# Kernel optimization log

Hardware: AMD Instinct MI355X
Metric: run time of the kernel (lower is better)

The kernel has to match this reference:

```python
import jax, jax.numpy as jnp
import numpy as np
import math

CTX_LEN = 2048
N_EMB = 256
HEAD_SIZE = 256
N_HEADS = 8
HEAD_DIM = HEAD_SIZE // N_HEADS  # 32
B, T = 4, 2048


def setup_inputs() -> dict:
    key = jax.random.key(0)
    k1, k2, k3, k4 = jax.random.split(key, 4)
    x = jax.random.normal(k1, (B, T, N_EMB), dtype=jnp.float32)
    # torch Linear(n_emb, 3*head_size, bias=False): store as [in, out] for x @ W
    w_attn = jax.random.normal(k2, (N_EMB, 3 * HEAD_SIZE), dtype=jnp.float32) * 0.02
    pos_embs = jax.random.normal(k3, (N_HEADS, CTX_LEN, HEAD_DIM), dtype=jnp.float32) * 0.02
    w_proj = jax.random.normal(k4, (HEAD_SIZE, N_EMB), dtype=jnp.float32) * 0.02
    b_proj = jnp.zeros((N_EMB,), dtype=jnp.float32)
    return {"x": x, "w_attn": w_attn, "pos_embs": pos_embs,
            "w_proj": w_proj, "b_proj": b_proj}


def reference(x, w_attn, pos_embs, w_proj, b_proj):
    Bsz, Tlen, _ = x.shape
    qkv = x @ w_attn                               # [B,T,3*HS]
    K, Q, V = jnp.split(qkv, 3, axis=-1)           # split order: K, Q, V (as in source)
    def heads(t):                                  # [B,T,HS] -> [B,H,T,hd]
        return t.reshape(Bsz, Tlen, N_HEADS, HEAD_DIM).transpose(0, 2, 1, 3)
    K, Q, V = heads(K), heads(Q), heads(V)

    # relative position term with skew trick
    pe = pos_embs[:, -Tlen:, :]                    # [H,T,hd]
    S_rel = jnp.einsum('bhtd,hsd->bhts', Q, pe)    # [B,H,T,T]
    flip_mask = jnp.flip(jnp.tril(jnp.ones((Tlen, Tlen), dtype=x.dtype)), axis=1)
    S_rel = S_rel * flip_mask
    # pad a zero column at the front, reshape [T+1,T], drop first row -> skew
    S_rel = jnp.pad(S_rel, ((0, 0), (0, 0), (0, 0), (1, 0)))
    S_rel = S_rel.reshape(Bsz, N_HEADS, Tlen + 1, Tlen)[:, :, 1:, :]

    scores = (jnp.einsum('bhtd,bhsd->bhts', Q, K) + S_rel) / math.sqrt(HEAD_DIM)
    causal = jnp.where(jnp.tril(jnp.ones((Tlen, Tlen), dtype=bool)), 0.0, -1e9).astype(x.dtype)
    scores = scores + causal
    attn = jax.nn.softmax(scores, axis=-1)         # dropout omitted (eval mode)

    out = jnp.einsum('bhts,bhsd->bhtd', attn, V)   # [B,H,T,hd]
    out = out.transpose(0, 2, 1, 3).reshape(Bsz, Tlen, HEAD_SIZE)
    return out @ w_proj + b_proj
```

## Files before the change

### kernel.cpp

```cpp
#include <hip/hip_runtime.h>
#include <math.h>

#define BB 4
#define TT 2048
#define NEMB 256
#define NH 8
#define HD 32

typedef __attribute__((ext_vector_type(8))) short bf8;
typedef __attribute__((ext_vector_type(4))) float f4;

static __device__ __forceinline__ unsigned short f2bf(float f) {
    union { float f; unsigned u; } v; v.f = f;
    unsigned r = v.u + 0x7FFF + ((v.u >> 16) & 1);
    return (unsigned short)(r >> 16);
}

__global__ __launch_bounds__(256) void xcvt(const float* __restrict__ x,
                                            unsigned short* __restrict__ xb) {
    const long i = (long)blockIdx.x * 256 + threadIdx.x;
    const float4 v = ((const float4*)x)[i];
    ushort4 o; o.x = f2bf(v.x); o.y = f2bf(v.y); o.z = f2bf(v.z); o.w = f2bf(v.w);
    ((ushort4*)xb)[i] = o;
}

__global__ __launch_bounds__(256) void tcvt(const float* __restrict__ src,
                                            unsigned short* __restrict__ dst,
                                            int R, int C) {
    __shared__ float t[64][65];
    const int tid = threadIdx.x;
    const int c0 = blockIdx.x * 64, r0 = blockIdx.y * 64;
    #pragma unroll
    for (int p = 0; p < 4; ++p) {
        const int i = tid + p * 256;
        const int r = i >> 4, c4 = (i & 15) * 4;
        const float4 v = *(const float4*)(src + (long)(r0 + r) * C + c0 + c4);
        t[r][c4] = v.x; t[r][c4+1] = v.y; t[r][c4+2] = v.z; t[r][c4+3] = v.w;
    }
    __syncthreads();
    #pragma unroll
    for (int p = 0; p < 4; ++p) {
        const int i = tid + p * 256;
        const int cr = i >> 4, r4 = (i & 15) * 4;
        ushort4 vv;
        vv.x = f2bf(t[r4+0][cr]); vv.y = f2bf(t[r4+1][cr]);
        vv.z = f2bf(t[r4+2][cr]); vv.w = f2bf(t[r4+3][cr]);
        *(ushort4*)(dst + (long)(c0 + cr) * R + r0 + r4) = vv;
    }
}

__global__ __launch_bounds__(256) void pe_cvt(const float* __restrict__ pe,
                                              unsigned short* __restrict__ peb) {
    const int i = blockIdx.x * 256 + threadIdx.x;
    const float4 v = ((const float4*)pe)[i];
    ushort4 o; o.x = f2bf(v.x); o.y = f2bf(v.y); o.z = f2bf(v.z); o.w = f2bf(v.w);
    ((ushort4*)peb)[i] = o;
}

__global__ __launch_bounds__(256) void qkv_mfma(const unsigned short* __restrict__ Ag,
                                                const unsigned short* __restrict__ Bg,
                                                unsigned short* __restrict__ Kb,
                                                unsigned short* __restrict__ Qb,
                                                unsigned short* __restrict__ Vt) {
    __shared__ unsigned short sm[13824];
    unsigned short* As = sm;
    unsigned short* Bs = sm + 9216;
    const int tid = threadIdx.x;
    const int wv = tid >> 6, L = tid & 63;
    const int l15 = L & 15, q = L >> 4;
    const int n0 = blockIdx.x * 64;
    const int m0 = blockIdx.y * 128;

    f4 acc[2][4];
    #pragma unroll
    for (int mt = 0; mt < 2; ++mt)
        #pragma unroll
        for (int nt = 0; nt < 4; ++nt) acc[mt][nt] = (f4){0.f,0.f,0.f,0.f};

    for (int kc = 0; kc < 4; ++kc) {
        const int k0 = kc * 64;
        __syncthreads();
        #pragma unroll
        for (int p = 0; p < 4; ++p) {
            const int i = tid + p * 256;
            const int r = i >> 3, c = i & 7;
            *(bf8*)(As + r * 72 + c * 8) = *(const bf8*)(Ag + (long)(m0 + r) * 256 + k0 + c * 8);
        }
        #pragma unroll
        for (int p = 0; p < 2; ++p) {
            const int i = tid + p * 256;
            const int r = i >> 3, c = i & 7;
            *(bf8*)(Bs + r * 72 + c * 8) = *(const bf8*)(Bg + (long)(n0 + r) * 256 + k0 + c * 8);
        }
        __syncthreads();
        #pragma unroll
        for (int kk = 0; kk < 2; ++kk) {
            const bf8 a0 = *(const bf8*)(As + (wv * 32 + l15) * 72 + kk * 32 + q * 8);
            const bf8 a1 = *(const bf8*)(As + (wv * 32 + 16 + l15) * 72 + kk * 32 + q * 8);
            #pragma unroll
            for (int nt = 0; nt < 4; ++nt) {
                const bf8 bb = *(const bf8*)(Bs + (nt * 16 + l15) * 72 + kk * 32 + q * 8);
                acc[0][nt] = __builtin_amdgcn_mfma_f32_16x16x32_bf16(a0, bb, acc[0][nt], 0, 0, 0);
                acc[1][nt] = __builtin_amdgcn_mfma_f32_16x16x32_bf16(a1, bb, acc[1][nt], 0, 0, 0);
            }
        }
    }

    const int sec = n0 >> 8;
    #pragma unroll
    for (int mt = 0; mt < 2; ++mt) {
        const int gm = m0 + wv * 32 + mt * 16 + q * 4;
        const int b = gm >> 11, tb = gm & 2047;
        #pragma unroll
        for (int nt = 0; nt < 4; ++nt) {
            const int gn = n0 + nt * 16 + l15;
            const int cc = gn & 255, h = cc >> 5, d = cc & 31;
            const long bh = (long)b * NH + h;
            const f4 a = acc[mt][nt];
            if (sec == 2) {
                ushort4 vv;
                vv.x = f2bf(a[0]); vv.y = f2bf(a[1]); vv.z = f2bf(a[2]); vv.w = f2bf(a[3]);
                *(ushort4*)(Vt + (bh * HD + d) * TT + tb) = vv;
            } else if (sec == 1) {
                #pragma unroll
                for (int r = 0; r < 4; ++r)
                    Qb[(bh * TT + tb + r) * HD + d] = f2bf(a[r] * 0.17677669529663687f);
            } else {
                #pragma unroll
                for (int r = 0; r < 4; ++r)
                    Kb[(bh * TT + tb + r) * HD + d] = f2bf(a[r]);
            }
        }
    }
}

__global__ __launch_bounds__(256) void attn_kernel(const unsigned short* __restrict__ Kb,
                                                   const unsigned short* __restrict__ Qb,
                                                   const unsigned short* __restrict__ Vtg,
                                                   const unsigned short* __restrict__ peb,
                                                   unsigned short* __restrict__ att) {
    __shared__ unsigned short lds[14592];
    unsigned short* Ks  = lds;
    unsigned short* PEs = lds + 2560;
    unsigned short* Vts = lds + 7680;
    unsigned short* Psw = lds + 9984 + (threadIdx.x >> 6) * 1152;

    const int tid = threadIdx.x;
    const int wv  = tid >> 6;
    const int L   = tid & 63;
    const int l15 = L & 15;
    const int q   = L >> 4;
    const int h = blockIdx.y, b = blockIdx.z;
    const long bh = (long)b * NH + h;
    const unsigned short* Kg = Kb  + bh * TT * HD;
    const unsigned short* Qg = Qb  + bh * TT * HD;
    const unsigned short* Vg = Vtg + bh * HD * TT;
    const unsigned short* Pg = peb + (long)h * TT * HD;

    const int krow = tid >> 2, kc = tid & 3;
    const int vrow = tid >> 3, vc = tid & 7;
    const f4 z4 = {0.f, 0.f, 0.f, 0.f};

    for (int half = 0; half < 2; ++half) {
        const int itile = half ? 31 - (int)blockIdx.x : (int)blockIdx.x;
        const int t0 = itile * 64;

        const bf8 aq = *(const bf8*)(Qg + (t0 + wv * 16 + l15) * HD + q * 8);
        f4 o0 = z4, o1 = z4;
        float m_st[4] = {-1e30f, -1e30f, -1e30f, -1e30f};
        float l_st[4] = {0.f, 0.f, 0.f, 0.f};

        for (int jt = 0; jt <= itile; ++jt) {
            const int s0 = jt * 64;
            const int ubase = TT - 64 - t0 + s0;
            __syncthreads();
            *(bf8*)(Ks  + krow * 40 + kc * 8) = *(const bf8*)(Kg + (s0 + krow) * HD + kc * 8);
            *(bf8*)(Vts + vrow * 72 + vc * 8) = *(const bf8*)(Vg + vrow * TT + s0 + vc * 8);
            #pragma unroll
            for (int kk = 0; kk < 2; ++kk) {
                const int i  = tid + kk * 256;
                const int pr = i >> 2, pc = i & 3;
                const int u  = ubase + pr;
                bf8 val = {0,0,0,0,0,0,0,0};
                if (u < TT) val = *(const bf8*)(Pg + (long)u * HD + pc * 8);
                *(bf8*)(PEs + pr * 40 + pc * 8) = val;
            }
            __syncthreads();

            f4 sa[4], ra[5];
            #pragma unroll
            for (int nt = 0; nt < 4; ++nt) {
                const bf8 bk = *(const bf8*)(Ks + (nt * 16 + l15) * 40 + q * 8);
                sa[nt] = __builtin_amdgcn_mfma_f32_16x16x32_bf16(aq, bk, z4, 0, 0, 0);
            }
            const int pebase = 48 - 16 * wv;
            #pragma unroll
            for (int nt = 0; nt < 5; ++nt) {
                const bf8 bp = *(const bf8*)(PEs + (pebase + nt * 16 + l15) * 40 + q * 8);
                ra[nt] = __builtin_amdgcn_mfma_f32_16x16x32_bf16(aq, bp, z4, 0, 0, 0);
            }

            #pragma unroll
            for (int nb = 0; nb < 4; ++nb) {
                #pragma unroll
                for (int r = 0; r < 4; ++r) {
                    const int shift = 15 - 4 * q - r;
                    const int tcol  = l15 + shift;
                    const int src   = (q << 4) | (tcol & 15);
                    const float va = __shfl(ra[nb][r], src);
                    const float vb = __shfl(ra[nb + 1][r], src);
                    sa[nb][r] += (tcol < 16) ? va : vb;
                }
            }

            if (jt == itile) {
                #pragma unroll
                for (int nb = 0; nb < 4; ++nb)
                    #pragma unroll
                    for (int r = 0; r < 4; ++r) {
                        const int s_l = nb * 16 + l15;
                        const int t_l = wv * 16 + 4 * q + r;
                        if (s_l > t_l) sa[nb][r] = -1e30f;
                    }
            }

            float corr[4];
            #pragma unroll
            for (int r = 0; r < 4; ++r) {
                float mx = fmaxf(fmaxf(sa[0][r], sa[1][r]), fmaxf(sa[2][r], sa[3][r]));
                mx = fmaxf(mx, __shfl_xor(mx, 1));
                mx = fmaxf(mx, __shfl_xor(mx, 2));
                mx = fmaxf(mx, __shfl_xor(mx, 4));
                mx = fmaxf(mx, __shfl_xor(mx, 8));
                const float mn = fmaxf(m_st[r], mx);
                corr[r] = __expf(m_st[r] - mn);
                m_st[r] = mn;
                float rs = 0.f;
                #pragma unroll
                for (int nb = 0; nb < 4; ++nb) {
                    const float p = __expf(sa[nb][r] - mn);
                    rs += p;
                    Psw[(4 * q + r) * 72 + nb * 16 + l15] = f2bf(p);
                }
                rs += __shfl_xor(rs, 1); rs += __shfl_xor(rs, 2);
                rs += __shfl_xor(rs, 4); rs += __shfl_xor(rs, 8);
                l_st[r] = l_st[r] * corr[r] + rs;
            }
            #pragma unroll
            for (int r = 0; r < 4; ++r) { o0[r] *= corr[r]; o1[r] *= corr[r]; }

            #pragma unroll
            for (int ks = 0; ks < 2; ++ks) {
                const bf8 ap  = *(const bf8*)(Psw + l15 * 72 + ks * 32 + q * 8);
                const bf8 bv0 = *(const bf8*)(Vts + l15 * 72 + ks * 32 + q * 8);
                const bf8 bv1 = *(const bf8*)(Vts + (16 + l15) * 72 + ks * 32 + q * 8);
                o0 = __builtin_amdgcn_mfma_f32_16x16x32_bf16(ap, bv0, o0, 0, 0, 0);
                o1 = __builtin_amdgcn_mfma_f32_16x16x32_bf16(ap, bv1, o1, 0, 0, 0);
            }
        }

        #pragma unroll
        for (int r = 0; r < 4; ++r) {
            const float inv = 1.0f / l_st[r];
            const int t = t0 + wv * 16 + 4 * q + r;
            unsigned short* dst = att + ((long)(b * TT + t)) * NEMB + h * HD;
            dst[l15]      = f2bf(o0[r] * inv);
            dst[16 + l15] = f2bf(o1[r] * inv);
        }
    }
}

__global__ __launch_bounds__(256) void proj_mfma(const unsigned short* __restrict__ Ag,
                                                 const unsigned short* __restrict__ Bg,
                                                 const float* __restrict__ bias,
                                                 float* __restrict__ out) {
    __shared__ unsigned short sm[13824];
    unsigned short* As = sm;
    unsigned short* Bs = sm + 9216;
    const int tid = threadIdx.x;
    const int wv = tid >> 6, L = tid & 63;
    const int l15 = L & 15, q = L >> 4;
    const int n0 = blockIdx.x * 64;
    const int m0 = blockIdx.y * 128;

    f4 acc[2][4];
    #pragma unroll
    for (int mt = 0; mt < 2; ++mt)
        #pragma unroll
        for (int nt = 0; nt < 4; ++nt) acc[mt][nt] = (f4){0.f,0.f,0.f,0.f};

    for (int kc = 0; kc < 4; ++kc) {
        const int k0 = kc * 64;
        __syncthreads();
        #pragma unroll
        for (int p = 0; p < 4; ++p) {
            const int i = tid + p * 256;
            const int r = i >> 3, c = i & 7;
            *(bf8*)(As + r * 72 + c * 8) = *(const bf8*)(Ag + (long)(m0 + r) * 256 + k0 + c * 8);
        }
        #pragma unroll
        for (int p = 0; p < 2; ++p) {
            const int i = tid + p * 256;
            const int r = i >> 3, c = i & 7;
            *(bf8*)(Bs + r * 72 + c * 8) = *(const bf8*)(Bg + (long)(n0 + r) * 256 + k0 + c * 8);
        }
        __syncthreads();
        #pragma unroll
        for (int kk = 0; kk < 2; ++kk) {
            const bf8 a0 = *(const bf8*)(As + (wv * 32 + l15) * 72 + kk * 32 + q * 8);
            const bf8 a1 = *(const bf8*)(As + (wv * 32 + 16 + l15) * 72 + kk * 32 + q * 8);
            #pragma unroll
            for (int nt = 0; nt < 4; ++nt) {
                const bf8 bb = *(const bf8*)(Bs + (nt * 16 + l15) * 72 + kk * 32 + q * 8);
                acc[0][nt] = __builtin_amdgcn_mfma_f32_16x16x32_bf16(a0, bb, acc[0][nt], 0, 0, 0);
                acc[1][nt] = __builtin_amdgcn_mfma_f32_16x16x32_bf16(a1, bb, acc[1][nt], 0, 0, 0);
            }
        }
    }

    #pragma unroll
    for (int mt = 0; mt < 2; ++mt) {
        const int gm = m0 + wv * 32 + mt * 16 + q * 4;
        #pragma unroll
        for (int nt = 0; nt < 4; ++nt) {
            const int gn = n0 + nt * 16 + l15;
            const float bv = bias[gn];
            #pragma unroll
            for (int r = 0; r < 4; ++r)
                out[(long)(gm + r) * NEMB + gn] = acc[mt][nt][r] + bv;
        }
    }
}

extern "C" void kernel_launch(void* const* d_in, const int* in_sizes, int n_in,
                              void* d_out, int out_size, void* d_ws, size_t ws_size,
                              hipStream_t stream) {
    const float* x      = (const float*)d_in[0];
    const float* w_attn = (const float*)d_in[1];
    const float* pe     = (const float*)d_in[2];
    const float* w_proj = (const float*)d_in[3];
    const float* b_proj = (const float*)d_in[4];
    float* out = (float*)d_out;

    char* base = (char*)d_ws;
    unsigned short* xb   = (unsigned short*)(base);
    unsigned short* Kb   = (unsigned short*)(base + ( 4u << 20));
    unsigned short* Qb   = (unsigned short*)(base + ( 8u << 20));
    unsigned short* Vt   = (unsigned short*)(base + (12u << 20));
    unsigned short* attb = (unsigned short*)(base + (16u << 20));
    unsigned short* peb  = (unsigned short*)(base + (20u << 20));
    unsigned short* waT  = (unsigned short*)(base + (21u << 20));
    unsigned short* wpT  = (unsigned short*)(base + (22u << 20));

    xcvt<<<dim3(2048), 256, 0, stream>>>(x, xb);
    tcvt<<<dim3(12, 4), 256, 0, stream>>>(w_attn, waT, NEMB, 768);
    tcvt<<<dim3(4, 4), 256, 0, stream>>>(w_proj, wpT, NEMB, NEMB);
    pe_cvt<<<dim3(512), 256, 0, stream>>>(pe, peb);
    qkv_mfma<<<dim3(12, 64), 256, 0, stream>>>(xb, waT, Kb, Qb, Vt);
    attn_kernel<<<dim3(16, NH, BB), 256, 0, stream>>>(Kb, Qb, Vt, peb, attb);
    proj_mfma<<<dim3(4, 64), 256, 0, stream>>>(attb, wpT, b_proj, out);
}
```

Measured before the change: 177.9 us.

## Fuse prep conversions, use DPP row reductions, exp2 softmax, packed bf16 skew shuffles

Merges the four conversion kernels into one launch to cut launch overhead. In attention, it folds log2(e) into the Q scale so softmax can use exp2f, swaps the shfl_xor row reductions for DPP moves, and packs the two relative-position values as bf16 into one 32-bit shuffle, halving the skew shuffles. Rounding the relative term to bf16 before adding it to the scores adds a small precision loss.

```diff
diff --git a/kernel.cpp b/kernel.cpp
--- a/kernel.cpp
+++ b/kernel.cpp
@@ -16,20 +16,30 @@
     return (unsigned short)(r >> 16);
 }
 
-__global__ __launch_bounds__(256) void xcvt(const float* __restrict__ x,
-                                            unsigned short* __restrict__ xb) {
-    const long i = (long)blockIdx.x * 256 + threadIdx.x;
-    const float4 v = ((const float4*)x)[i];
-    ushort4 o; o.x = f2bf(v.x); o.y = f2bf(v.y); o.z = f2bf(v.z); o.w = f2bf(v.w);
-    ((ushort4*)xb)[i] = o;
-}
-
-__global__ __launch_bounds__(256) void tcvt(const float* __restrict__ src,
-                                            unsigned short* __restrict__ dst,
-                                            int R, int C) {
-    __shared__ float t[64][65];
-    const int tid = threadIdx.x;
-    const int c0 = blockIdx.x * 64, r0 = blockIdx.y * 64;
+template <int CTRL>
+static __device__ __forceinline__ float dppmv(float x) {
+    return __int_as_float(__builtin_amdgcn_mov_dpp(__float_as_int(x), CTRL, 0xF, 0xF, true));
+}
+static __device__ __forceinline__ float rowmax16(float x) {
+    x = fmaxf(x, dppmv<0xB1>(x));
+    x = fmaxf(x, dppmv<0x4E>(x));
+    x = fmaxf(x, dppmv<0x124>(x));
+    x = fmaxf(x, dppmv<0x128>(x));
+    return x;
+}
+static __device__ __forceinline__ float rowsum16(float x) {
+    x += dppmv<0xB1>(x);
+    x += dppmv<0x4E>(x);
+    x += dppmv<0x124>(x);
+    x += dppmv<0x128>(x);
+    return x;
+}
+
+static __device__ __forceinline__ void tcvt_body(const float* __restrict__ src,
+                                                 unsigned short* __restrict__ dst,
+                                                 int R, int C, int gx, int gy,
+                                                 float (*t)[65], int tid) {
+    const int c0 = gx * 64, r0 = gy * 64;
     #pragma unroll
     for (int p = 0; p < 4; ++p) {
         const int i = tid + p * 256;
@@ -49,12 +59,33 @@
     }
 }
 
-__global__ __launch_bounds__(256) void pe_cvt(const float* __restrict__ pe,
-                                              unsigned short* __restrict__ peb) {
-    const int i = blockIdx.x * 256 + threadIdx.x;
-    const float4 v = ((const float4*)pe)[i];
-    ushort4 o; o.x = f2bf(v.x); o.y = f2bf(v.y); o.z = f2bf(v.z); o.w = f2bf(v.w);
-    ((ushort4*)peb)[i] = o;
+__global__ __launch_bounds__(256) void prep(const float* __restrict__ x,
+                                            unsigned short* __restrict__ xb,
+                                            const float* __restrict__ pe,
+                                            unsigned short* __restrict__ peb,
+                                            const float* __restrict__ wa,
+                                            unsigned short* __restrict__ waT,
+                                            const float* __restrict__ wp,
+                                            unsigned short* __restrict__ wpT) {
+    __shared__ float t[64][65];
+    const int bx = blockIdx.x, tid = threadIdx.x;
+    if (bx < 2048) {
+        const long i = (long)bx * 256 + tid;
+        const float4 v = ((const float4*)x)[i];
+        ushort4 o; o.x = f2bf(v.x); o.y = f2bf(v.y); o.z = f2bf(v.z); o.w = f2bf(v.w);
+        ((ushort4*)xb)[i] = o;
+    } else if (bx < 2560) {
+        const long i = (long)(bx - 2048) * 256 + tid;
+        const float4 v = ((const float4*)pe)[i];
+        ushort4 o; o.x = f2bf(v.x); o.y = f2bf(v.y); o.z = f2bf(v.z); o.w = f2bf(v.w);
+        ((ushort4*)peb)[i] = o;
+    } else if (bx < 2608) {
+        const int lo = bx - 2560;
+        tcvt_body(wa, waT, 256, 768, lo % 12, lo / 12, t, tid);
+    } else {
+        const int lo = bx - 2608;
+        tcvt_body(wp, wpT, 256, 256, lo % 4, lo / 4, t, tid);
+    }
 }
 
 __global__ __launch_bounds__(256) void qkv_mfma(const unsigned short* __restrict__ Ag,
@@ -124,7 +155,7 @@
             } else if (sec == 1) {
                 #pragma unroll
                 for (int r = 0; r < 4; ++r)
-                    Qb[(bh * TT + tb + r) * HD + d] = f2bf(a[r] * 0.17677669529663687f);
+                    Qb[(bh * TT + tb + r) * HD + d] = f2bf(a[r] * 0.25506655788696527f);
             } else {
                 #pragma unroll
                 for (int r = 0; r < 4; ++r)
@@ -200,16 +231,22 @@
                 ra[nt] = __builtin_amdgcn_mfma_f32_16x16x32_bf16(aq, bp, z4, 0, 0, 0);
             }
 
+            unsigned short rb[5][4];
+            #pragma unroll
+            for (int nt = 0; nt < 5; ++nt)
+                #pragma unroll
+                for (int r = 0; r < 4; ++r) rb[nt][r] = f2bf(ra[nt][r]);
             #pragma unroll
             for (int nb = 0; nb < 4; ++nb) {
                 #pragma unroll
                 for (int r = 0; r < 4; ++r) {
+                    const unsigned packed = (unsigned)rb[nb][r] | ((unsigned)rb[nb + 1][r] << 16);
                     const int shift = 15 - 4 * q - r;
                     const int tcol  = l15 + shift;
                     const int src   = (q << 4) | (tcol & 15);
-                    const float va = __shfl(ra[nb][r], src);
-                    const float vb = __shfl(ra[nb + 1][r], src);
-                    sa[nb][r] += (tcol < 16) ? va : vb;
+                    const unsigned v = (unsigned)__shfl((int)packed, src);
+                    const unsigned sel = (tcol < 16) ? (v << 16) : (v & 0xFFFF0000u);
+                    sa[nb][r] += __int_as_float((int)sel);
                 }
             }
 
@@ -228,22 +265,18 @@
             #pragma unroll
             for (int r = 0; r < 4; ++r) {
                 float mx = fmaxf(fmaxf(sa[0][r], sa[1][r]), fmaxf(sa[2][r], sa[3][r]));
-                mx = fmaxf(mx, __shfl_xor(mx, 1));
-                mx = fmaxf(mx, __shfl_xor(mx, 2));
-                mx = fmaxf(mx, __shfl_xor(mx, 4));
-                mx = fmaxf(mx, __shfl_xor(mx, 8));
+                mx = rowmax16(mx);
                 const float mn = fmaxf(m_st[r], mx);
-                corr[r] = __expf(m_st[r] - mn);
+                corr[r] = exp2f(m_st[r] - mn);
                 m_st[r] = mn;
                 float rs = 0.f;
                 #pragma unroll
                 for (int nb = 0; nb < 4; ++nb) {
-                    const float p = __expf(sa[nb][r] - mn);
+                    const float p = exp2f(sa[nb][r] - mn);
                     rs += p;
                     Psw[(4 * q + r) * 72 + nb * 16 + l15] = f2bf(p);
                 }
-                rs += __shfl_xor(rs, 1); rs += __shfl_xor(rs, 2);
-                rs += __shfl_xor(rs, 4); rs += __shfl_xor(rs, 8);
+                rs = rowsum16(rs);
                 l_st[r] = l_st[r] * corr[r] + rs;
             }
             #pragma unroll
@@ -352,10 +385,7 @@
     unsigned short* waT  = (unsigned short*)(base + (21u << 20));
     unsigned short* wpT  = (unsigned short*)(base + (22u << 20));
 
-    xcvt<<<dim3(2048), 256, 0, stream>>>(x, xb);
-    tcvt<<<dim3(12, 4), 256, 0, stream>>>(w_attn, waT, NEMB, 768);
-    tcvt<<<dim3(4, 4), 256, 0, stream>>>(w_proj, wpT, NEMB, NEMB);
-    pe_cvt<<<dim3(512), 256, 0, stream>>>(pe, peb);
+    prep<<<dim3(2624), 256, 0, stream>>>(x, xb, pe, peb, w_attn, waT, w_proj, wpT);
     qkv_mfma<<<dim3(12, 64), 256, 0, stream>>>(xb, waT, Kb, Qb, Vt);
     attn_kernel<<<dim3(16, NH, BB), 256, 0, stream>>>(Kb, Qb, Vt, peb, attb);
     proj_mfma<<<dim3(4, 64), 256, 0, stream>>>(attb, wpT, b_proj, out);
```

Result: faster. 169.1 us (-5.0%).
